# Optimization experiments

Measured on AMD Instinct MI355X. Metric: run time of the kernel, lower is better.

Reference implementation:

```python
import jax, jax.numpy as jnp
import numpy as np

HIDDEN = 1280
HEADS = 16
HEAD_DIM = HIDDEN // HEADS  # 80
INTER = 4608
DEPTH = 4
WIN = 64                     # tokens per attention window
FULL_BLOCKS = (3,)           # fullatt_block_indexes
EPS = 1e-6
SEQ = 3072


def setup_inputs() -> dict:
    key = jax.random.key(0)
    ks = jax.random.split(key, 20)
    sc = lambda *s: 0.02
    inp = {
        "x": jax.random.normal(ks[0], (SEQ, HIDDEN), jnp.float32),
        "rotary_pos_emb": jax.random.uniform(ks[1], (SEQ, HEAD_DIM // 2), jnp.float32) * 3.0,
        "s_aux": jax.random.normal(ks[2], (HEADS,), jnp.float32),
        "ln1_w": jnp.ones((DEPTH, HIDDEN), jnp.float32),
        "ln1_b": jnp.zeros((DEPTH, HIDDEN), jnp.float32),
        "qkv_w": jax.random.normal(ks[3], (DEPTH, HIDDEN, 3 * HIDDEN), jnp.float32) * 0.02,
        "qkv_b": jnp.zeros((DEPTH, 3 * HIDDEN), jnp.float32),
        "proj_w": jax.random.normal(ks[4], (DEPTH, HIDDEN, HIDDEN), jnp.float32) * 0.02,
        "proj_b": jnp.zeros((DEPTH, HIDDEN), jnp.float32),
        "ln2_w": jnp.ones((DEPTH, HIDDEN), jnp.float32),
        "ln2_b": jnp.zeros((DEPTH, HIDDEN), jnp.float32),
        "gate_w": jax.random.normal(ks[5], (DEPTH, HIDDEN, INTER), jnp.float32) * 0.02,
        "gate_b": jnp.zeros((DEPTH, INTER), jnp.float32),
        "up_w": jax.random.normal(ks[6], (DEPTH, HIDDEN, INTER), jnp.float32) * 0.02,
        "up_b": jnp.zeros((DEPTH, INTER), jnp.float32),
        "down_w": jax.random.normal(ks[7], (DEPTH, INTER, HIDDEN), jnp.float32) * 0.02,
        "down_b": jnp.zeros((DEPTH, HIDDEN), jnp.float32),
    }
    return inp


def _layer_norm(x, w, b):
    mu = jnp.mean(x, axis=-1, keepdims=True)
    var = jnp.mean(jnp.square(x - mu), axis=-1, keepdims=True)
    return (x - mu) * jax.lax.rsqrt(var + EPS) * w + b


def _rotate_half(x):
    x1, x2 = jnp.split(x, 2, axis=-1)
    return jnp.concatenate([-x2, x1], axis=-1)


def _apply_rotary(q, k, rot):
    # q,k: [S, H, D]; rot: [S, D/2]
    emb = jnp.concatenate([rot, rot], axis=-1)          # [S, D]
    cos = jnp.cos(emb)[:, None, :]
    sin = jnp.sin(emb)[:, None, :]
    q = q * cos + _rotate_half(q) * sin
    k = k * cos + _rotate_half(k) * sin
    return q, k


def _attention_with_sinks(q, k, v, s_aux):
    # q,k,v: [B, T, H, D]; block-diagonal within each of B windows.
    scale = 1.0 / jnp.sqrt(jnp.asarray(HEAD_DIM, q.dtype))
    scores = jnp.einsum("bqhd,bkhd->bhqk", q, k) * scale      # [B,H,q,k]
    sink = s_aux[None, :, None]                                # [1,H,1]
    m = jnp.maximum(jnp.max(scores, axis=-1), sink)            # [B,H,q]
    p = jnp.exp(scores - m[..., None])                         # [B,H,q,k]
    denom = jnp.sum(p, axis=-1) + jnp.exp(sink - m)            # [B,H,q]
    out = jnp.einsum("bhqk,bkhd->bqhd", p, v)
    out = out / jnp.transpose(denom, (0, 2, 1))[..., None]     # [B,q,H,D]
    return out


def reference(x, rotary_pos_emb, s_aux, ln1_w, ln1_b, qkv_w, qkv_b, proj_w, proj_b,
              ln2_w, ln2_b, gate_w, gate_b, up_w, up_b, down_w, down_b):
    S = x.shape[0]
    h = x
    for l in range(DEPTH):
        # --- attention ---
        hn = _layer_norm(h, ln1_w[l], ln1_b[l])
        qkv = hn @ qkv_w[l] + qkv_b[l]                          # [S, 3*HIDDEN]
        qkv = qkv.reshape(S, 3, HEADS, HEAD_DIM)
        q, k, v = qkv[:, 0], qkv[:, 1], qkv[:, 2]               # [S,H,D]
        q, k = _apply_rotary(q, k, rotary_pos_emb)
        if l in FULL_BLOCKS:
            B, T = 1, S                                         # full attention
        else:
            B, T = S // WIN, WIN                                # windowed (varlen block-diag)
        qw = q.reshape(B, T, HEADS, HEAD_DIM)
        kw = k.reshape(B, T, HEADS, HEAD_DIM)
        vw = v.reshape(B, T, HEADS, HEAD_DIM)
        o = _attention_with_sinks(qw, kw, vw, s_aux)            # [B,T,H,D]
        o = o.reshape(S, HIDDEN) @ proj_w[l] + proj_b[l]
        h = h + o
        # --- gated SiLU MLP ---
        hn = _layer_norm(h, ln2_w[l], ln2_b[l])
        g = jax.nn.silu(hn @ gate_w[l] + gate_b[l]) * (hn @ up_w[l] + up_b[l])
        h = h + g @ down_w[l] + down_b[l]
    return h
```

## Files before the change

kernel.cpp:

```cpp
#include <hip/hip_runtime.h>
#include <math.h>

typedef unsigned short u16;
typedef unsigned int u32;

using bf16x8 = __attribute__((ext_vector_type(8))) __bf16;
using f32x4  = __attribute__((ext_vector_type(4))) float;

#define SEQ 3072
#define HID 1280
#define NHEADS 16
#define HDIM 80
#define INTER 4608

#define LOG2E 1.44269504088896f
#define M2C   11.5415603f

__device__ __forceinline__ u16 f2bf(float f) {
    union { float f; u32 u; } v; v.f = f;
    u32 u = v.u;
    u32 r = u + 0x7fffu + ((u >> 16) & 1u);
    return (u16)(r >> 16);
}

__device__ __forceinline__ void gld16(const void* g, void* l) {
    __builtin_amdgcn_global_load_lds((const __attribute__((address_space(1))) void*)g,
                                     (__attribute__((address_space(3))) void*)l,
                                     16, 0, 0);
}

__device__ __forceinline__ bf16x8 frag8(const u16* base, int row, int ks, int quad) {
    int c = ks * 4 + quad;
    return *(const bf16x8*)&base[(row * 8 + (c ^ (row & 7))) * 8];
}

__global__ __launch_bounds__(256) void transpose_pack(const float* __restrict__ src,
                                                      u16* __restrict__ dst, int K, int N) {
    __shared__ float tile[32][33];
    int l = blockIdx.z;
    const float* s = src + (size_t)l * K * N;
    u16* d = dst + (size_t)l * N * K;
    int n0 = blockIdx.x * 32, k0 = blockIdx.y * 32;
    int tx = threadIdx.x & 31, ty = threadIdx.x >> 5;
#pragma unroll
    for (int i = 0; i < 4; i++) {
        int k = ty + i * 8;
        tile[k][tx] = s[(size_t)(k0 + k) * N + n0 + tx];
    }
    __syncthreads();
#pragma unroll
    for (int i = 0; i < 4; i++) {
        int n = ty + i * 8;
        d[(size_t)(n0 + n) * K + k0 + tx] = f2bf(tile[tx][n]);
    }
}

__global__ __launch_bounds__(256) void ln_kernel(const float* __restrict__ x,
                                                 const float* __restrict__ w,
                                                 const float* __restrict__ b,
                                                 u16* __restrict__ out) {
    int row = blockIdx.x;
    const float* xr = x + (size_t)row * HID;
    float v[5]; float s = 0.f, s2 = 0.f;
#pragma unroll
    for (int i = 0; i < 5; i++) { float t = xr[threadIdx.x + i * 256]; v[i] = t; s += t; s2 += t * t; }
#pragma unroll
    for (int off = 32; off > 0; off >>= 1) { s += __shfl_down(s, off); s2 += __shfl_down(s2, off); }
    __shared__ float red[8];
    int wv = threadIdx.x >> 6;
    if ((threadIdx.x & 63) == 0) { red[wv] = s; red[wv + 4] = s2; }
    __syncthreads();
    s  = red[0] + red[1] + red[2] + red[3];
    s2 = red[4] + red[5] + red[6] + red[7];
    float mu  = s * (1.f / HID);
    float var = s2 * (1.f / HID) - mu * mu;
    float rstd = rsqrtf(var + 1e-6f);
#pragma unroll
    for (int i = 0; i < 5; i++) {
        int col = threadIdx.x + i * 256;
        out[(size_t)row * HID + col] = f2bf((v[i] - mu) * rstd * w[col] + b[col]);
    }
}

__global__ __launch_bounds__(256) void qkv_pack(const float* __restrict__ qkv,
                                                const float* __restrict__ rot,
                                                u16* __restrict__ Qp, u16* __restrict__ Kp,
                                                u16* __restrict__ Vt) {
    const float QSC = 0.111803398874989485f * LOG2E;
    int s0 = blockIdx.x * 64, h = blockIdx.y;
    int tid = threadIdx.x;
    __shared__ u16 vlds[80 * 66];
    for (int idx = tid; idx < 64 * 40; idx += 256) {
        int r = idx / 40, d = idx - r * 40;
        const float* base = qkv + (size_t)(s0 + r) * 3840 + h * 80;
        float sn, cs;
        __sincosf(rot[(size_t)(s0 + r) * 40 + d], &sn, &cs);
        float q1 = base[d], q2 = base[d + 40];
        float k1 = base[1280 + d], k2 = base[1280 + d + 40];
        size_t ro = ((size_t)h * SEQ + s0 + r) * 128;
        Qp[ro + d]      = f2bf((q1 * cs - q2 * sn) * QSC);
        Qp[ro + d + 40] = f2bf((q2 * cs + q1 * sn) * QSC);
        Kp[ro + d]      = f2bf(k1 * cs - k2 * sn);
        Kp[ro + d + 40] = f2bf(k2 * cs + k1 * sn);
    }
    for (int idx = tid; idx < 64 * 48; idx += 256) {
        int r = idx / 48, d = 80 + (idx - r * 48);
        size_t ro = ((size_t)h * SEQ + s0 + r) * 128;
        Qp[ro + d] = 0; Kp[ro + d] = 0;
    }
    for (int idx = tid; idx < 64 * 80; idx += 256) {
        int r = idx / 80, d = idx - r * 80;
        vlds[d * 66 + r] = f2bf(qkv[(size_t)(s0 + r) * 3840 + 2560 + h * 80 + d]);
    }
    __syncthreads();
    for (int idx = tid; idx < 80 * 64; idx += 256) {
        int d = idx >> 6, ky = idx & 63;
        Vt[((size_t)h * 80 + d) * SEQ + s0 + ky] = vlds[d * 66 + ky];
    }
}

template<int MODE>
__global__ __launch_bounds__(256) void gemm_v3(const u16* __restrict__ A,
                                               const u16* __restrict__ B0,
                                               const u16* __restrict__ B1,
                                               const float* __restrict__ bias0,
                                               const float* __restrict__ bias1,
                                               const float* __restrict__ res,
                                               float* __restrict__ outf,
                                               u16* __restrict__ outh,
                                               int N, int K, int sx, int sy) {
    __shared__ u16 As[8192];
    __shared__ u16 Bs[(MODE == 1) ? 4096 : 8192];
    int tid = threadIdx.x, lane = tid & 63, wave = tid >> 6;
    int quad = lane >> 4, r15 = lane & 15;
    int f = blockIdx.x, xcd = f & 7, j = f >> 3;
    int bx, by;
    if (sx) { bx = xcd * sx + j % sx; by = j / sx; }
    else    { by = xcd * sy + j % sy; bx = j / sy; }
    int mBase = by * 128;
    int nBase = (MODE == 0) ? bx * 128 : bx * 64;

    int rs = tid >> 3, cs = tid & 7;
    int c0 = cs ^ (rs & 7);
    const u16* gA = A + (size_t)(mBase + rs) * K + c0 * 8;
    const u16* gB0 = B0 + (size_t)(nBase + rs) * K + c0 * 8;
    const u16* gB1 = (MODE == 2) ? (B1 + (size_t)(nBase + rs) * K + c0 * 8) : nullptr;
    u16* dA = &As[(wave * 64) * 8];

    f32x4 acc[MODE == 0 ? 4 : 2][4] = {};
    f32x4 acu[MODE == 2 ? 2 : 1][4] = {};

    int wm = wave >> 1, wn = wave & 1;
    int nK = K >> 6;
    for (int kt = 0; kt < nK; kt++) {
        const u16* a = gA + kt * 64;
        const u16* b0 = gB0 + kt * 64;
#pragma unroll
        for (int i = 0; i < 4; i++)
            gld16(a + (size_t)(i * 32) * K, dA + i * 2048);
        if constexpr (MODE == 0) {
#pragma unroll
            for (int i = 0; i < 4; i++)
                gld16(b0 + (size_t)(i * 32) * K, &Bs[(wave * 64) * 8 + i * 2048]);
        } else if constexpr (MODE == 1) {
#pragma unroll
            for (int i = 0; i < 2; i++)
                gld16(b0 + (size_t)(i * 32) * K, &Bs[(wave * 64) * 8 + i * 2048]);
        } else {
            const u16* b1 = gB1 + kt * 64;
#pragma unroll
            for (int i = 0; i < 2; i++)
                gld16(b0 + (size_t)(i * 32) * K, &Bs[(wave * 64) * 8 + i * 2048]);
#pragma unroll
            for (int i = 0; i < 2; i++)
                gld16(b1 + (size_t)(i * 32) * K, &Bs[4096 + (wave * 64) * 8 + i * 2048]);
        }
        __syncthreads();

#pragma unroll
        for (int ks = 0; ks < 2; ks++) {
            if constexpr (MODE == 0) {
                bf16x8 af[4], bf[4];
#pragma unroll
                for (int mi = 0; mi < 4; mi++) af[mi] = frag8(As, wm * 64 + mi * 16 + r15, ks, quad);
#pragma unroll
                for (int ni = 0; ni < 4; ni++) bf[ni] = frag8(Bs, wn * 64 + ni * 16 + r15, ks, quad);
#pragma unroll
                for (int mi = 0; mi < 4; mi++)
#pragma unroll
                    for (int ni = 0; ni < 4; ni++)
                        acc[mi][ni] = __builtin_amdgcn_mfma_f32_16x16x32_bf16(af[mi], bf[ni], acc[mi][ni], 0, 0, 0);
            } else if constexpr (MODE == 1) {
                bf16x8 af[2], bf[4];
#pragma unroll
                for (int mi = 0; mi < 2; mi++) af[mi] = frag8(As, wave * 32 + mi * 16 + r15, ks, quad);
#pragma unroll
                for (int ni = 0; ni < 4; ni++) bf[ni] = frag8(Bs, ni * 16 + r15, ks, quad);
#pragma unroll
                for (int mi = 0; mi < 2; mi++)
#pragma unroll
                    for (int ni = 0; ni < 4; ni++)
                        acc[mi][ni] = __builtin_amdgcn_mfma_f32_16x16x32_bf16(af[mi], bf[ni], acc[mi][ni], 0, 0, 0);
            } else {
                bf16x8 af[2];
#pragma unroll
                for (int mi = 0; mi < 2; mi++) af[mi] = frag8(As, wave * 32 + mi * 16 + r15, ks, quad);
#pragma unroll
                for (int ni = 0; ni < 4; ni++) {
                    bf16x8 bg = frag8(Bs, ni * 16 + r15, ks, quad);
                    bf16x8 bu = frag8(Bs + 4096, ni * 16 + r15, ks, quad);
#pragma unroll
                    for (int mi = 0; mi < 2; mi++) {
                        acc[mi][ni] = __builtin_amdgcn_mfma_f32_16x16x32_bf16(af[mi], bg, acc[mi][ni], 0, 0, 0);
                        acu[mi][ni] = __builtin_amdgcn_mfma_f32_16x16x32_bf16(af[mi], bu, acu[mi][ni], 0, 0, 0);
                    }
                }
            }
        }
        __syncthreads();
    }

    if constexpr (MODE == 0) {
#pragma unroll
        for (int ni = 0; ni < 4; ni++) {
            int col = nBase + wn * 64 + ni * 16 + r15;
            float bv = bias0[col];
#pragma unroll
            for (int mi = 0; mi < 4; mi++)
#pragma unroll
                for (int jj = 0; jj < 4; jj++) {
                    int row = mBase + wm * 64 + mi * 16 + quad * 4 + jj;
                    outf[(size_t)row * N + col] = acc[mi][ni][jj] + bv;
                }
        }
    } else if constexpr (MODE == 1) {
#pragma unroll
        for (int ni = 0; ni < 4; ni++) {
            int col = nBase + ni * 16 + r15;
            float bv = bias0[col];
#pragma unroll
            for (int mi = 0; mi < 2; mi++)
#pragma unroll
                for (int jj = 0; jj < 4; jj++) {
                    int row = mBase + wave * 32 + mi * 16 + quad * 4 + jj;
                    outf[(size_t)row * N + col] = acc[mi][ni][jj] + bv + res[(size_t)row * N + col];
                }
        }
    } else {
#pragma unroll
        for (int ni = 0; ni < 4; ni++) {
            int col = nBase + ni * 16 + r15;
            float gb = bias0[col], ub = bias1[col];
#pragma unroll
            for (int mi = 0; mi < 2; mi++)
#pragma unroll
                for (int jj = 0; jj < 4; jj++) {
                    int row = mBase + wave * 32 + mi * 16 + quad * 4 + jj;
                    float g = acc[mi][ni][jj] + gb;
                    float u = acu[mi][ni][jj] + ub;
                    float sg = g / (1.f + __expf(-g));
                    outh[(size_t)row * INTER + col] = f2bf(sg * u);
                }
        }
    }
}

__global__ __launch_bounds__(256) void attn_kernel(const u16* __restrict__ Qp,
                                                   const u16* __restrict__ Kp,
                                                   const u16* __restrict__ Vt,
                                                   const float* __restrict__ s_aux,
                                                   u16* __restrict__ out, int windowed) {
    __shared__ u16 q_lds[8192];
    __shared__ u16 k_lds[8192];
    __shared__ u16 v_lds[5120];
    __shared__ u16 p_lds[64 * 72];

    int qt = blockIdx.x, h = blockIdx.y;
    int tid = threadIdx.x, lane = tid & 63, wave = tid >> 6;
    int quad = lane >> 4, r15 = lane & 15;

    const u16* Qh = Qp + (size_t)h * SEQ * 128;
    const u16* Kh = Kp + (size_t)h * SEQ * 128;
    const u16* Vh = Vt + (size_t)h * 80 * SEQ;

    {
        int q0 = qt * 64;
#pragma unroll
        for (int i = 0; i < 4; i++) {
            int slot = i * 256 + wave * 64 + lane;
            int row = slot >> 4, cc = slot & 15;
            int c = cc ^ (row & 7);
            gld16(Qh + (size_t)(q0 + row) * 128 + c * 8, &q_lds[(i * 256 + wave * 64) * 8]);
        }
    }
    __syncthreads();
    bf16x8 aq[3];
#pragma unroll
    for (int ks = 0; ks < 3; ks++) {
        int row = wave * 16 + r15;
        int c = ks * 4 + quad;
        aq[ks] = *(const bf16x8*)&q_lds[(row * 16 + (c ^ (row & 7))) * 8];
    }

    float l_j[4] = {0.f, 0.f, 0.f, 0.f};
    f32x4 ov[5] = {};

    int nT = windowed ? 1 : (SEQ / 64);
    int tBase = windowed ? qt : 0;
    for (int t = 0; t < nT; t++) {
        int key0 = (tBase + t) * 64;
        __syncthreads();
#pragma unroll
        for (int i = 0; i < 4; i++) {
            int slot = i * 256 + wave * 64 + lane;
            int row = slot >> 4, cc = slot & 15;
            int c = cc ^ (row & 7);
            gld16(Kh + (size_t)(key0 + row) * 128 + c * 8, &k_lds[(i * 256 + wave * 64) * 8]);
        }
#pragma unroll
        for (int i = 0; i < 2; i++) {
            int slot = i * 256 + wave * 64 + lane;
            int row = slot >> 3, cc = slot & 7;
            int c = cc ^ (row & 7);
            gld16(Vh + (size_t)row * SEQ + key0 + c * 8, &v_lds[(i * 256 + wave * 64) * 8]);
        }
        if (wave < 2) {
            int slot = 512 + wave * 64 + lane;
            int row = slot >> 3, cc = slot & 7;
            int c = cc ^ (row & 7);
            gld16(Vh + (size_t)row * SEQ + key0 + c * 8, &v_lds[(512 + wave * 64) * 8]);
        }
        __syncthreads();

        f32x4 sc[4];
#pragma unroll
        for (int nt = 0; nt < 4; nt++) {
            f32x4 z = {};
#pragma unroll
            for (int ks = 0; ks < 3; ks++) {
                int row = nt * 16 + r15;
                int c = ks * 4 + quad;
                bf16x8 bk = *(const bf16x8*)&k_lds[(row * 16 + (c ^ (row & 7))) * 8];
                z = __builtin_amdgcn_mfma_f32_16x16x32_bf16(aq[ks], bk, z, 0, 0, 0);
            }
            sc[nt] = z;
        }
#pragma unroll
        for (int nt = 0; nt < 4; nt++)
#pragma unroll
            for (int jj = 0; jj < 4; jj++) {
                float p = __builtin_amdgcn_exp2f(sc[nt][jj] - M2C);
                l_j[jj] += p;
                p_lds[(wave * 16 + quad * 4 + jj) * 72 + nt * 16 + r15] = f2bf(p);
            }
        asm volatile("s_waitcnt lgkmcnt(0)" ::: "memory");
        bf16x8 ap[2];
#pragma unroll
        for (int ks = 0; ks < 2; ks++)
            ap[ks] = *(const bf16x8*)&p_lds[(wave * 16 + r15) * 72 + ks * 32 + quad * 8];
#pragma unroll
        for (int t5 = 0; t5 < 5; t5++)
#pragma unroll
            for (int ks = 0; ks < 2; ks++) {
                int d = t5 * 16 + r15;
                int c = ks * 4 + quad;
                bf16x8 bv = *(const bf16x8*)&v_lds[(d * 8 + (c ^ (d & 7))) * 8];
                ov[t5] = __builtin_amdgcn_mfma_f32_16x16x32_bf16(ap[ks], bv, ov[t5], 0, 0, 0);
            }
    }
#pragma unroll
    for (int off = 1; off < 16; off <<= 1)
#pragma unroll
        for (int jj = 0; jj < 4; jj++)
            l_j[jj] += __shfl_xor(l_j[jj], off, 64);
    float sink = s_aux[h];
    float se = __builtin_amdgcn_exp2f(sink * LOG2E - M2C);
#pragma unroll
    for (int jj = 0; jj < 4; jj++) l_j[jj] = 1.f / (l_j[jj] + se);
#pragma unroll
    for (int t5 = 0; t5 < 5; t5++)
#pragma unroll
        for (int jj = 0; jj < 4; jj++) {
            int row = qt * 64 + wave * 16 + quad * 4 + jj;
            int d = t5 * 16 + r15;
            out[(size_t)row * HID + h * 80 + d] = f2bf(ov[t5][jj] * l_j[jj]);
        }
}

__global__ __launch_bounds__(256) void copy4_kernel(const float4* __restrict__ src,
                                                    float4* __restrict__ dst) {
    size_t i = (size_t)blockIdx.x * 256 + threadIdx.x;
    dst[i] = src[i];
}

extern "C" void kernel_launch(void* const* d_in, const int* in_sizes, int n_in,
                              void* d_out, int out_size, void* d_ws, size_t ws_size,
                              hipStream_t stream) {
    const float* x      = (const float*)d_in[0];
    const float* rot    = (const float*)d_in[1];
    const float* s_aux  = (const float*)d_in[2];
    const float* ln1_w  = (const float*)d_in[3];
    const float* ln1_b  = (const float*)d_in[4];
    const float* qkv_w  = (const float*)d_in[5];
    const float* qkv_b  = (const float*)d_in[6];
    const float* proj_w = (const float*)d_in[7];
    const float* proj_b = (const float*)d_in[8];
    const float* ln2_w  = (const float*)d_in[9];
    const float* ln2_b  = (const float*)d_in[10];
    const float* gate_w = (const float*)d_in[11];
    const float* gate_b = (const float*)d_in[12];
    const float* up_w   = (const float*)d_in[13];
    const float* up_b   = (const float*)d_in[14];
    const float* down_w = (const float*)d_in[15];
    const float* down_b = (const float*)d_in[16];

    char* ws = (char*)d_ws;
    size_t off = 0;
    auto alloc = [&](size_t n) -> char* {
        char* p = ws + off; off += (n + 255) & ~(size_t)255; return p;
    };
    u16* wt_qkv  = (u16*)alloc((size_t)4 * 3840 * 1280 * 2);
    u16* wt_proj = (u16*)alloc((size_t)4 * 1280 * 1280 * 2);
    u16* wt_gate = (u16*)alloc((size_t)4 * 4608 * 1280 * 2);
    u16* wt_up   = (u16*)alloc((size_t)4 * 4608 * 1280 * 2);
    u16* wt_down = (u16*)alloc((size_t)4 * 1280 * 4608 * 2);
    float* h     = (float*)alloc((size_t)3072 * 1280 * 4);
    u16*  xn     = (u16*)alloc((size_t)3072 * 1280 * 2);
    float* gbuf  = (float*)alloc((size_t)3072 * 4608 * 4);
    float* qkvb  = gbuf;
    u16*  attnb  = (u16*)alloc((size_t)3072 * 1280 * 2);
    float* ubuf  = (float*)alloc((size_t)3072 * 4608 * 4);
    u16*  mbuf   = (u16*)alloc((size_t)3072 * 4608 * 2);
    u16* Qp  = (u16*)ubuf;
    u16* Kp  = Qp + (size_t)NHEADS * SEQ * 128;
    u16* Vtp = Kp + (size_t)NHEADS * SEQ * 128;

    transpose_pack<<<dim3(120, 40, 4), 256, 0, stream>>>(qkv_w,  wt_qkv,  1280, 3840);
    transpose_pack<<<dim3(40,  40, 4), 256, 0, stream>>>(proj_w, wt_proj, 1280, 1280);
    transpose_pack<<<dim3(144, 40, 4), 256, 0, stream>>>(gate_w, wt_gate, 1280, 4608);
    transpose_pack<<<dim3(144, 40, 4), 256, 0, stream>>>(up_w,   wt_up,   1280, 4608);
    transpose_pack<<<dim3(40, 144, 4), 256, 0, stream>>>(down_w, wt_down, 4608, 1280);

    copy4_kernel<<<3840, 256, 0, stream>>>((const float4*)x, (float4*)h);

    for (int l = 0; l < 4; l++) {
        ln_kernel<<<3072, 256, 0, stream>>>(h, ln1_w + l * 1280, ln1_b + l * 1280, xn);
        gemm_v3<0><<<720, 256, 0, stream>>>(xn, wt_qkv + (size_t)l * 3840 * 1280, nullptr,
                                            qkv_b + l * 3840, nullptr, nullptr, qkvb, nullptr,
                                            3840, 1280, 0, 3);
        qkv_pack<<<dim3(48, 16), 256, 0, stream>>>(qkvb, rot, Qp, Kp, Vtp);
        attn_kernel<<<dim3(48, 16), 256, 0, stream>>>(Qp, Kp, Vtp, s_aux, attnb, (l == 3) ? 0 : 1);
        gemm_v3<1><<<480, 256, 0, stream>>>(attnb, wt_proj + (size_t)l * 1280 * 1280, nullptr,
                                            proj_b + l * 1280, nullptr, h, h, nullptr,
                                            1280, 1280, 0, 3);
        ln_kernel<<<3072, 256, 0, stream>>>(h, ln2_w + l * 1280, ln2_b + l * 1280, xn);
        gemm_v3<2><<<1728, 256, 0, stream>>>(xn, wt_gate + (size_t)l * 4608 * 1280,
                                             wt_up + (size_t)l * 4608 * 1280,
                                             gate_b + l * 4608, up_b + l * 4608, nullptr,
                                             nullptr, mbuf, 4608, 1280, 9, 0);
        float* outp = (l == 3) ? (float*)d_out : h;
        gemm_v3<1><<<480, 256, 0, stream>>>(mbuf, wt_down + (size_t)l * 4608 * 1280, nullptr,
                                            down_b + l * 1280, nullptr, h, outp, nullptr,
                                            1280, 4608, 0, 3);
    }
}
```

Measured before the change: 1.751 ms.

## Add 256x256 double-buffered GEMM with interleaved gate/up weights for QKV and MLP

Introduces a new 512-thread GEMM kernel with 256x256 output tiles, double-buffered LDS staging that prefetches the next K tile between MFMA phases, and setprio around the MFMA blocks. Gate and up weights are repacked into one interleaved matrix (16-column groups alternating), so the fused SiLU-gated MLP becomes a single GEMM with the activation in its epilogue. QKV and gate/up projections switch to this kernel, while proj and down keep a simplified gemm_v3 that now only supports the residual mode. Larger tiles raise data reuse and cut global traffic, at the cost of fewer workgroups (180 for QKV) and heavy register and LDS use (128KB per block).

```diff
diff --git a/kernel.cpp b/kernel.cpp
--- a/kernel.cpp
+++ b/kernel.cpp
@@ -52,6 +52,30 @@
     for (int i = 0; i < 4; i++) {
         int n = ty + i * 8;
         d[(size_t)(n0 + n) * K + k0 + tx] = f2bf(tile[tx][n]);
+    }
+}
+
+__global__ __launch_bounds__(256) void transpose_pack_gu(const float* __restrict__ src,
+                                                         u16* __restrict__ dst, int K, int N,
+                                                         int which) {
+    __shared__ float tile[32][33];
+    int l = blockIdx.z;
+    const float* s = src + (size_t)l * K * N;
+    u16* d = dst + (size_t)l * (2 * N) * K;
+    int n0 = blockIdx.x * 32, k0 = blockIdx.y * 32;
+    int tx = threadIdx.x & 31, ty = threadIdx.x >> 5;
+#pragma unroll
+    for (int i = 0; i < 4; i++) {
+        int k = ty + i * 8;
+        tile[k][tx] = s[(size_t)(k0 + k) * N + n0 + tx];
+    }
+    __syncthreads();
+#pragma unroll
+    for (int i = 0; i < 4; i++) {
+        int n = ty + i * 8;
+        int g = n0 + n;
+        int n2 = ((g >> 4) << 5) | (g & 15) | (which << 4);
+        d[(size_t)n2 * K + k0 + tx] = f2bf(tile[tx][n]);
     }
 }
 
@@ -144,13 +168,10 @@
     int c0 = cs ^ (rs & 7);
     const u16* gA = A + (size_t)(mBase + rs) * K + c0 * 8;
     const u16* gB0 = B0 + (size_t)(nBase + rs) * K + c0 * 8;
-    const u16* gB1 = (MODE == 2) ? (B1 + (size_t)(nBase + rs) * K + c0 * 8) : nullptr;
     u16* dA = &As[(wave * 64) * 8];
 
     f32x4 acc[MODE == 0 ? 4 : 2][4] = {};
-    f32x4 acu[MODE == 2 ? 2 : 1][4] = {};
-
-    int wm = wave >> 1, wn = wave & 1;
+
     int nK = K >> 6;
     for (int kt = 0; kt < nK; kt++) {
         const u16* a = gA + kt * 64;
@@ -158,106 +179,141 @@
 #pragma unroll
         for (int i = 0; i < 4; i++)
             gld16(a + (size_t)(i * 32) * K, dA + i * 2048);
-        if constexpr (MODE == 0) {
-#pragma unroll
-            for (int i = 0; i < 4; i++)
-                gld16(b0 + (size_t)(i * 32) * K, &Bs[(wave * 64) * 8 + i * 2048]);
-        } else if constexpr (MODE == 1) {
-#pragma unroll
-            for (int i = 0; i < 2; i++)
-                gld16(b0 + (size_t)(i * 32) * K, &Bs[(wave * 64) * 8 + i * 2048]);
-        } else {
-            const u16* b1 = gB1 + kt * 64;
-#pragma unroll
-            for (int i = 0; i < 2; i++)
-                gld16(b0 + (size_t)(i * 32) * K, &Bs[(wave * 64) * 8 + i * 2048]);
-#pragma unroll
-            for (int i = 0; i < 2; i++)
-                gld16(b1 + (size_t)(i * 32) * K, &Bs[4096 + (wave * 64) * 8 + i * 2048]);
-        }
+#pragma unroll
+        for (int i = 0; i < 2; i++)
+            gld16(b0 + (size_t)(i * 32) * K, &Bs[(wave * 64) * 8 + i * 2048]);
         __syncthreads();
 
 #pragma unroll
         for (int ks = 0; ks < 2; ks++) {
-            if constexpr (MODE == 0) {
-                bf16x8 af[4], bf[4];
-#pragma unroll
-                for (int mi = 0; mi < 4; mi++) af[mi] = frag8(As, wm * 64 + mi * 16 + r15, ks, quad);
-#pragma unroll
-                for (int ni = 0; ni < 4; ni++) bf[ni] = frag8(Bs, wn * 64 + ni * 16 + r15, ks, quad);
-#pragma unroll
-                for (int mi = 0; mi < 4; mi++)
-#pragma unroll
-                    for (int ni = 0; ni < 4; ni++)
-                        acc[mi][ni] = __builtin_amdgcn_mfma_f32_16x16x32_bf16(af[mi], bf[ni], acc[mi][ni], 0, 0, 0);
-            } else if constexpr (MODE == 1) {
-                bf16x8 af[2], bf[4];
-#pragma unroll
-                for (int mi = 0; mi < 2; mi++) af[mi] = frag8(As, wave * 32 + mi * 16 + r15, ks, quad);
-#pragma unroll
-                for (int ni = 0; ni < 4; ni++) bf[ni] = frag8(Bs, ni * 16 + r15, ks, quad);
-#pragma unroll
-                for (int mi = 0; mi < 2; mi++)
-#pragma unroll
-                    for (int ni = 0; ni < 4; ni++)
-                        acc[mi][ni] = __builtin_amdgcn_mfma_f32_16x16x32_bf16(af[mi], bf[ni], acc[mi][ni], 0, 0, 0);
-            } else {
-                bf16x8 af[2];
-#pragma unroll
-                for (int mi = 0; mi < 2; mi++) af[mi] = frag8(As, wave * 32 + mi * 16 + r15, ks, quad);
-#pragma unroll
-                for (int ni = 0; ni < 4; ni++) {
-                    bf16x8 bg = frag8(Bs, ni * 16 + r15, ks, quad);
-                    bf16x8 bu = frag8(Bs + 4096, ni * 16 + r15, ks, quad);
-#pragma unroll
-                    for (int mi = 0; mi < 2; mi++) {
-                        acc[mi][ni] = __builtin_amdgcn_mfma_f32_16x16x32_bf16(af[mi], bg, acc[mi][ni], 0, 0, 0);
-                        acu[mi][ni] = __builtin_amdgcn_mfma_f32_16x16x32_bf16(af[mi], bu, acu[mi][ni], 0, 0, 0);
-                    }
-                }
+            bf16x8 af[2], bf[4];
+#pragma unroll
+            for (int mi = 0; mi < 2; mi++) af[mi] = frag8(As, wave * 32 + mi * 16 + r15, ks, quad);
+#pragma unroll
+            for (int ni = 0; ni < 4; ni++) bf[ni] = frag8(Bs, ni * 16 + r15, ks, quad);
+#pragma unroll
+            for (int mi = 0; mi < 2; mi++)
+#pragma unroll
+                for (int ni = 0; ni < 4; ni++)
+                    acc[mi][ni] = __builtin_amdgcn_mfma_f32_16x16x32_bf16(af[mi], bf[ni], acc[mi][ni], 0, 0, 0);
+        }
+        __syncthreads();
+    }
+
+#pragma unroll
+    for (int ni = 0; ni < 4; ni++) {
+        int col = nBase + ni * 16 + r15;
+        float bv = bias0[col];
+#pragma unroll
+        for (int mi = 0; mi < 2; mi++)
+#pragma unroll
+            for (int jj = 0; jj < 4; jj++) {
+                int row = mBase + wave * 32 + mi * 16 + quad * 4 + jj;
+                outf[(size_t)row * N + col] = acc[mi][ni][jj] + bv + res[(size_t)row * N + col];
             }
-        }
-        __syncthreads();
-    }
-
-    if constexpr (MODE == 0) {
+    }
+}
+
+template<int EPI>
+__global__ __launch_bounds__(512, 2) void gemm8(const u16* __restrict__ A,
+                                                const u16* __restrict__ B,
+                                                const float* __restrict__ bias0,
+                                                const float* __restrict__ bias1,
+                                                float* __restrict__ outf,
+                                                u16* __restrict__ outh,
+                                                int N, int K) {
+    __shared__ u16 sbuf[65536];
+    int tid = threadIdx.x, lane = tid & 63, wave = tid >> 6;
+    int quad = lane >> 4, r15 = lane & 15;
+    int wm = wave >> 2, wn = wave & 3;
+
+    int nwg = gridDim.x;
+    int q8 = nwg >> 3, r8 = nwg & 7;
+    int xcd = blockIdx.x & 7, j = blockIdx.x >> 3;
+    int wg = (xcd < r8 ? xcd * (q8 + 1) : r8 * (q8 + 1) + (xcd - r8) * q8) + j;
+    int bx = wg / 12, by = wg % 12;
+    int mBase = by * 256, nBase = bx * 256;
+
+    int rs = tid >> 3, cs = tid & 7;
+    int c0 = cs ^ (rs & 7);
+    const u16* gA = A + (size_t)(mBase + rs) * K + c0 * 8;
+    const u16* gB = B + (size_t)(nBase + rs) * K + c0 * 8;
+    int nK = K >> 6;
+
+    f32x4 acc[8][4] = {};
+
+    auto stage = [&](int bi, int kt, int p) {
+        const u16* g = (p < 2) ? (gA + (size_t)kt * 64) : (gB + (size_t)kt * 64);
+        int i0 = (p & 1) * 2;
+        u16* d = &sbuf[bi * 32768 + ((p >= 2) ? 16384 : 0) + wave * 512 + i0 * 4096];
+        gld16(g + (size_t)(i0 * 64) * K, d);
+        gld16(g + (size_t)((i0 + 1) * 64) * K, d + 4096);
+    };
+
+#pragma unroll
+    for (int p = 0; p < 4; p++) stage(0, 0, p);
+    asm volatile("s_waitcnt vmcnt(0)" ::: "memory");
+    __builtin_amdgcn_s_barrier();
+
+    for (int kt = 0; kt < nK; kt++) {
+        int cur = kt & 1;
+        const u16* Ab = &sbuf[cur * 32768];
+        const u16* Bb = &sbuf[cur * 32768 + 16384];
+        bool pre = (kt + 1 < nK);
+        bf16x8 bfr[4];
+#pragma unroll
+        for (int p = 0; p < 4; p++) {
+            const int ks = p >> 1, mh = p & 1;
+            bf16x8 af[4];
+#pragma unroll
+            for (int qi = 0; qi < 4; qi++)
+                af[qi] = frag8(Ab, wm * 128 + mh * 64 + qi * 16 + r15, ks, quad);
+            if ((p & 1) == 0) {
+#pragma unroll
+                for (int ni = 0; ni < 4; ni++)
+                    bfr[ni] = frag8(Bb, wn * 64 + ni * 16 + r15, ks, quad);
+            }
+            if (pre) stage(cur ^ 1, kt + 1, p);
+            __builtin_amdgcn_s_barrier();
+            __builtin_amdgcn_s_setprio(1);
+#pragma unroll
+            for (int qi = 0; qi < 4; qi++)
+#pragma unroll
+                for (int ni = 0; ni < 4; ni++)
+                    acc[mh * 4 + qi][ni] = __builtin_amdgcn_mfma_f32_16x16x32_bf16(
+                        af[qi], bfr[ni], acc[mh * 4 + qi][ni], 0, 0, 0);
+            __builtin_amdgcn_s_setprio(0);
+            if (p < 3) __builtin_amdgcn_s_barrier();
+        }
+        if (pre) { asm volatile("s_waitcnt vmcnt(0)" ::: "memory"); }
+        __builtin_amdgcn_s_barrier();
+    }
+
+    if constexpr (EPI == 0) {
 #pragma unroll
         for (int ni = 0; ni < 4; ni++) {
             int col = nBase + wn * 64 + ni * 16 + r15;
             float bv = bias0[col];
 #pragma unroll
-            for (int mi = 0; mi < 4; mi++)
+            for (int mi = 0; mi < 8; mi++)
 #pragma unroll
                 for (int jj = 0; jj < 4; jj++) {
-                    int row = mBase + wm * 64 + mi * 16 + quad * 4 + jj;
+                    int row = mBase + wm * 128 + mi * 16 + quad * 4 + jj;
                     outf[(size_t)row * N + col] = acc[mi][ni][jj] + bv;
                 }
         }
-    } else if constexpr (MODE == 1) {
-#pragma unroll
-        for (int ni = 0; ni < 4; ni++) {
-            int col = nBase + ni * 16 + r15;
-            float bv = bias0[col];
-#pragma unroll
-            for (int mi = 0; mi < 2; mi++)
+    } else {
+#pragma unroll
+        for (int pp = 0; pp < 2; pp++) {
+            int col = (nBase >> 1) + wn * 32 + pp * 16 + r15;
+            float gb = bias0[col], ub = bias1[col];
+#pragma unroll
+            for (int mi = 0; mi < 8; mi++)
 #pragma unroll
                 for (int jj = 0; jj < 4; jj++) {
-                    int row = mBase + wave * 32 + mi * 16 + quad * 4 + jj;
-                    outf[(size_t)row * N + col] = acc[mi][ni][jj] + bv + res[(size_t)row * N + col];
-                }
-        }
-    } else {
-#pragma unroll
-        for (int ni = 0; ni < 4; ni++) {
-            int col = nBase + ni * 16 + r15;
-            float gb = bias0[col], ub = bias1[col];
-#pragma unroll
-            for (int mi = 0; mi < 2; mi++)
-#pragma unroll
-                for (int jj = 0; jj < 4; jj++) {
-                    int row = mBase + wave * 32 + mi * 16 + quad * 4 + jj;
-                    float g = acc[mi][ni][jj] + gb;
-                    float u = acu[mi][ni][jj] + ub;
+                    int row = mBase + wm * 128 + mi * 16 + quad * 4 + jj;
+                    float g = acc[mi][2 * pp][jj] + gb;
+                    float u = acc[mi][2 * pp + 1][jj] + ub;
                     float sg = g / (1.f + __expf(-g));
                     outh[(size_t)row * INTER + col] = f2bf(sg * u);
                 }
@@ -421,8 +477,7 @@
     };
     u16* wt_qkv  = (u16*)alloc((size_t)4 * 3840 * 1280 * 2);
     u16* wt_proj = (u16*)alloc((size_t)4 * 1280 * 1280 * 2);
-    u16* wt_gate = (u16*)alloc((size_t)4 * 4608 * 1280 * 2);
-    u16* wt_up   = (u16*)alloc((size_t)4 * 4608 * 1280 * 2);
+    u16* wt_gu   = (u16*)alloc((size_t)4 * 9216 * 1280 * 2);
     u16* wt_down = (u16*)alloc((size_t)4 * 1280 * 4608 * 2);
     float* h     = (float*)alloc((size_t)3072 * 1280 * 4);
     u16*  xn     = (u16*)alloc((size_t)3072 * 1280 * 2);
@@ -437,27 +492,26 @@
 
     transpose_pack<<<dim3(120, 40, 4), 256, 0, stream>>>(qkv_w,  wt_qkv,  1280, 3840);
     transpose_pack<<<dim3(40,  40, 4), 256, 0, stream>>>(proj_w, wt_proj, 1280, 1280);
-    transpose_pack<<<dim3(144, 40, 4), 256, 0, stream>>>(gate_w, wt_gate, 1280, 4608);
-    transpose_pack<<<dim3(144, 40, 4), 256, 0, stream>>>(up_w,   wt_up,   1280, 4608);
+    transpose_pack_gu<<<dim3(144, 40, 4), 256, 0, stream>>>(gate_w, wt_gu, 1280, 4608, 0);
+    transpose_pack_gu<<<dim3(144, 40, 4), 256, 0, stream>>>(up_w,   wt_gu, 1280, 4608, 1);
     transpose_pack<<<dim3(40, 144, 4), 256, 0, stream>>>(down_w, wt_down, 4608, 1280);
 
     copy4_kernel<<<3840, 256, 0, stream>>>((const float4*)x, (float4*)h);
 
     for (int l = 0; l < 4; l++) {
         ln_kernel<<<3072, 256, 0, stream>>>(h, ln1_w + l * 1280, ln1_b + l * 1280, xn);
-        gemm_v3<0><<<720, 256, 0, stream>>>(xn, wt_qkv + (size_t)l * 3840 * 1280, nullptr,
-                                            qkv_b + l * 3840, nullptr, nullptr, qkvb, nullptr,
-                                            3840, 1280, 0, 3);
+        gemm8<0><<<180, 512, 0, stream>>>(xn, wt_qkv + (size_t)l * 3840 * 1280,
+                                          qkv_b + l * 3840, nullptr, qkvb, nullptr,
+                                          3840, 1280);
         qkv_pack<<<dim3(48, 16), 256, 0, stream>>>(qkvb, rot, Qp, Kp, Vtp);
         attn_kernel<<<dim3(48, 16), 256, 0, stream>>>(Qp, Kp, Vtp, s_aux, attnb, (l == 3) ? 0 : 1);
         gemm_v3<1><<<480, 256, 0, stream>>>(attnb, wt_proj + (size_t)l * 1280 * 1280, nullptr,
                                             proj_b + l * 1280, nullptr, h, h, nullptr,
                                             1280, 1280, 0, 3);
         ln_kernel<<<3072, 256, 0, stream>>>(h, ln2_w + l * 1280, ln2_b + l * 1280, xn);
-        gemm_v3<2><<<1728, 256, 0, stream>>>(xn, wt_gate + (size_t)l * 4608 * 1280,
-                                             wt_up + (size_t)l * 4608 * 1280,
-                                             gate_b + l * 4608, up_b + l * 4608, nullptr,
-                                             nullptr, mbuf, 4608, 1280, 9, 0);
+        gemm8<2><<<432, 512, 0, stream>>>(xn, wt_gu + (size_t)l * 9216 * 1280,
+                                          gate_b + l * 4608, up_b + l * 4608,
+                                          nullptr, mbuf, 9216, 1280);
         float* outp = (l == 3) ? (float*)d_out : h;
         gemm_v3<1><<<480, 256, 0, stream>>>(mbuf, wt_down + (size_t)l * 4608 * 1280, nullptr,
                                             down_b + l * 1280, nullptr, h, outp, nullptr,
```

Measured after the change: 1.651 ms. -5.7%, faster.
